# Performance work log

Measured on AMD Instinct MI355X. Metric: run time of the kernel, lower is better.

Reference implementation:

```python
import jax, jax.numpy as jnp
import numpy as np

D = 1024   # dims
H = 16     # heads
HD = D // H  # head_dim = 64
F = HD // 2  # rotary frequency count


def _layernorm(x, g, b, eps=1e-5):
    m = x.mean(-1, keepdims=True)
    v = jnp.mean((x - m) ** 2, axis=-1, keepdims=True)
    return (x - m) * jax.lax.rsqrt(v + eps) * g + b


def _freq_base():
    # mask=None branch of rotary._compute_freqs: mel-style frequencies
    mel_max = 2595.0 * np.log10(1.0 + 4000.0 / 200.0)
    scale = 10.0 ** (np.linspace(0.0, mel_max, F) / 2595.0) - 1.0
    return jnp.asarray(200.0 * scale / 1000.0, dtype=jnp.float32)  # [F]


def _rope_polar(xh, radius, theta):
    # xh: [b,h,c,hd]; radius: [b,c] (learned per-token magnitude); theta: [c,F]
    # complex multiply of interleaved pairs by r*exp(i*theta)
    b_, h_, c_, hd_ = xh.shape
    xp = xh.reshape(b_, h_, c_, F, 2)
    xr, xi = xp[..., 0], xp[..., 1]
    cos = jnp.cos(theta)[None, None]  # [1,1,c,F]
    sin = jnp.sin(theta)[None, None]
    r = radius[:, None, :, None]      # [b,1,c,1]
    out_r = r * (xr * cos - xi * sin)
    out_i = r * (xr * sin + xi * cos)
    return jnp.stack([out_r, out_i], axis=-1).reshape(b_, h_, c_, hd_)


def setup_inputs() -> dict:
    key = jax.random.key(0)
    ks = jax.random.split(key, 6)
    B, C = 2, 2048
    s = 0.02
    return {
        "x": jax.random.normal(ks[0], (B, C, D), jnp.float32),
        "ln_q_g": jnp.ones((D,), jnp.float32),
        "ln_q_b": jnp.zeros((D,), jnp.float32),
        "Wq": jax.random.normal(ks[1], (D, D), jnp.float32) * s,
        "bq": jnp.zeros((D,), jnp.float32),
        "ln_kv_g": jnp.ones((D,), jnp.float32),
        "ln_kv_b": jnp.zeros((D,), jnp.float32),
        "Wkv": jax.random.normal(ks[2], (D, 2 * D), jnp.float32) * s,
        "bkv": jnp.zeros((2 * D,), jnp.float32),
        "Wout": jax.random.normal(ks[3], (D, D), jnp.float32) * s,
        "bout": jnp.zeros((D,), jnp.float32),
        "lnh_g": jnp.ones((HD,), jnp.float32),
        "lnh_b": jnp.zeros((HD,), jnp.float32),
        "Wr": jax.random.normal(ks[4], (D, 1), jnp.float32) * s,
        "br": jnp.zeros((1,), jnp.float32),
    }


def reference(x, ln_q_g, ln_q_b, Wq, bq, ln_kv_g, ln_kv_b, Wkv, bkv,
              Wout, bout, lnh_g, lnh_b, Wr, br):
    B, C, _ = x.shape
    # q path: norm -> linear -> [b,h,c,d]
    q = (_layernorm(x, ln_q_g, ln_q_b) @ Wq + bq).reshape(B, C, H, HD).transpose(0, 2, 1, 3)
    # kv path: norm -> linear -> [2,b,h,c,d]
    kv = (_layernorm(x, ln_kv_g, ln_kv_b) @ Wkv + bkv).reshape(B, C, 2, H, HD).transpose(2, 0, 3, 1, 4)
    k, v = kv[0], kv[1]
    # polar RoPE with learned per-token radius (xa = x for both q and k)
    t = jnp.arange(C, dtype=jnp.float32)
    theta = t[:, None] * _freq_base()[None, :]               # [C,F]
    per_step = (x @ Wr + br)[..., 0]                         # [B,C]
    radius = jnp.clip(per_step / 100.0, 0.5, 2.0)
    q = _rope_polar(q, radius, theta)
    k = _rope_polar(k, radius, theta)
    # per-head LayerNorm fused into SDPA inputs
    qn = _layernorm(q, lnh_g, lnh_b)
    kn = _layernorm(k, lnh_g, lnh_b)
    # non-causal SDPA (torch default scale = 1/sqrt(head_dim))
    logits = jnp.einsum('bhqd,bhkd->bhqk', qn, kn) / jnp.sqrt(jnp.float32(HD))
    attn = jax.nn.softmax(logits, axis=-1)
    o = jnp.einsum('bhqk,bhkd->bhqd', attn, v)
    o = o.transpose(0, 2, 1, 3).reshape(B, C, D)
    return o @ Wout + bout
```

## Files before the change

kernel.cpp:

```cpp
#include <hip/hip_runtime.h>
#include <math.h>

#define D_MODEL 1024
#define NHEADS  16
#define HEADD   64
#define NFREQ   32
#define BATCH   2
#define CSEQ    2048
#define NROWS   (BATCH*CSEQ)

typedef _Float16 half8  __attribute__((ext_vector_type(8)));
typedef _Float16 half4v __attribute__((ext_vector_type(4)));
typedef float    f32x4  __attribute__((ext_vector_type(4)));

__device__ __forceinline__ void async16(void* lds, const void* g)
{
    __builtin_amdgcn_global_load_lds((const __attribute__((address_space(1))) unsigned int*)g,
                                     (__attribute__((address_space(3))) unsigned int*)lds,
                                     16, 0, 0);
}

__global__ __launch_bounds__(256) void build_cs_kernel(float2* __restrict__ cs)
{
    int i = blockIdx.x * 256 + threadIdx.x;
    if (i >= CSEQ * NFREQ) return;
    int c = i >> 5, f = i & (NFREQ - 1);
    double mel_max = 2595.0 * log10(21.0);
    double step    = mel_max / (double)(NFREQ - 1);
    double freq    = 200.0 * (pow(10.0, step * (double)f / 2595.0) - 1.0) / 1000.0;
    float fr = (float)freq;
    float th = (float)c * fr;
    float s, co;
    sincosf(th, &s, &co);
    cs[i] = make_float2(co, s);
}

__global__ __launch_bounds__(256) void transpose_cast_kernel(
    const float* __restrict__ in, _Float16* __restrict__ out, int R, int C)
{
    __shared__ float t[32][33];
    int bx = blockIdx.x * 32;
    int by = blockIdx.y * 32;
    int tx = threadIdx.x, ty = threadIdx.y;
    #pragma unroll
    for (int i = ty; i < 32; i += 8)
        t[i][tx] = in[(size_t)(by + i) * C + bx + tx];
    __syncthreads();
    #pragma unroll
    for (int i = ty; i < 32; i += 8)
        out[(size_t)(bx + i) * R + by + tx] = (_Float16)t[tx][i];
}

__global__ __launch_bounds__(256) void ln_radius_kernel(
    const float* __restrict__ x,
    const float* __restrict__ gq,  const float* __restrict__ bq,
    const float* __restrict__ gkv, const float* __restrict__ bkv,
    const float* __restrict__ Wr,  const float* __restrict__ br,
    _Float16* __restrict__ xq, _Float16* __restrict__ xkv,
    float* __restrict__ radius)
{
    int row = blockIdx.x;
    int tid = threadIdx.x;
    float4 xv = ((const float4*)(x + (size_t)row * D_MODEL))[tid];
    float4 wv = ((const float4*)Wr)[tid];
    float s  = xv.x + xv.y + xv.z + xv.w;
    float ss = xv.x*xv.x + xv.y*xv.y + xv.z*xv.z + xv.w*xv.w;
    float dr = xv.x*wv.x + xv.y*wv.y + xv.z*wv.z + xv.w*wv.w;
    #pragma unroll
    for (int off = 1; off < 64; off <<= 1) {
        s  += __shfl_xor(s, off);
        ss += __shfl_xor(ss, off);
        dr += __shfl_xor(dr, off);
    }
    __shared__ float red[3][4];
    int w = tid >> 6, lane = tid & 63;
    if (lane == 0) { red[0][w] = s; red[1][w] = ss; red[2][w] = dr; }
    __syncthreads();
    s  = red[0][0] + red[0][1] + red[0][2] + red[0][3];
    ss = red[1][0] + red[1][1] + red[1][2] + red[1][3];
    float mean = s * (1.f / D_MODEL);
    float var  = ss * (1.f / D_MODEL) - mean * mean;
    float rinv = rsqrtf(var + 1e-5f);
    float4 gqv = ((const float4*)gq)[tid],  bqv = ((const float4*)bq)[tid];
    float4 gkv4= ((const float4*)gkv)[tid], bkv4= ((const float4*)bkv)[tid];
    float xn0 = (xv.x - mean) * rinv, xn1 = (xv.y - mean) * rinv;
    float xn2 = (xv.z - mean) * rinv, xn3 = (xv.w - mean) * rinv;
    half4v q4 = { (_Float16)(xn0*gqv.x + bqv.x), (_Float16)(xn1*gqv.y + bqv.y),
                  (_Float16)(xn2*gqv.z + bqv.z), (_Float16)(xn3*gqv.w + bqv.w) };
    half4v k4 = { (_Float16)(xn0*gkv4.x + bkv4.x), (_Float16)(xn1*gkv4.y + bkv4.y),
                  (_Float16)(xn2*gkv4.z + bkv4.z), (_Float16)(xn3*gkv4.w + bkv4.w) };
    *(half4v*)&xq [(size_t)row * D_MODEL + tid * 4] = q4;
    *(half4v*)&xkv[(size_t)row * D_MODEL + tid * 4] = k4;
    if (tid == 0) {
        float drt = red[2][0] + red[2][1] + red[2][2] + red[2][3];
        float p = (drt + br[0]) * 0.01f;
        radius[row] = fminf(fmaxf(p, 0.5f), 2.0f);
    }
}

__device__ __forceinline__ void gemm_core64(
    const _Float16* __restrict__ A, const _Float16* __restrict__ B,
    int bm, int bn, int K, _Float16* As, _Float16* Bs, f32x4 (*acc)[4])
{
    int tid = threadIdx.x, lane = tid & 63, w = tid >> 6;
    int wm = w >> 1, wn = w & 1;
    int l15 = lane & 15, lg = lane >> 4;
    int sr8 = lane >> 3;
    int csrc = (lane & 7) ^ sr8;

    auto stage = [&](int buf, int k0) {
        #pragma unroll
        for (int i = 0; i < 4; ++i) {
            int seg = w * 4 + i;
            int row = seg * 8 + sr8;
            async16(&As[buf * 8192 + seg * 512], &A[(size_t)(bm + row) * K + k0 + csrc * 8]);
            async16(&Bs[buf * 8192 + seg * 512], &B[(size_t)(bn + row) * K + k0 + csrc * 8]);
        }
    };

    stage(0, 0);
    __syncthreads();
    int cur = 0;
    for (int k0 = 0; k0 < K; k0 += 64) {
        if (k0 + 64 < K) stage(cur ^ 1, k0 + 64);
        #pragma unroll
        for (int ks = 0; ks < 2; ++ks) {
            half8 af[4], bf[4];
            #pragma unroll
            for (int m = 0; m < 4; ++m) {
                int row = wm * 64 + m * 16 + l15;
                af[m] = *(const half8*)&As[cur * 8192 + row * 64 + ((ks * 4 + lg) ^ (row & 7)) * 8];
            }
            #pragma unroll
            for (int n = 0; n < 4; ++n) {
                int row = wn * 64 + n * 16 + l15;
                bf[n] = *(const half8*)&Bs[cur * 8192 + row * 64 + ((ks * 4 + lg) ^ (row & 7)) * 8];
            }
            #pragma unroll
            for (int m = 0; m < 4; ++m)
                #pragma unroll
                for (int n = 0; n < 4; ++n)
                    acc[m][n] = __builtin_amdgcn_mfma_f32_16x16x32_f16(af[m], bf[n], acc[m][n], 0, 0, 0);
        }
        __syncthreads();
        cur ^= 1;
    }
}

__global__ __launch_bounds__(256) void gemm_qkv_kernel(
    const _Float16* __restrict__ xq,  const _Float16* __restrict__ xkv,
    const _Float16* __restrict__ WqT, const _Float16* __restrict__ WkvT,
    const float* __restrict__ bq,     const float* __restrict__ bkv,
    const float* __restrict__ radius, const float2* __restrict__ cs_tab,
    const float* __restrict__ lnh_g,  const float* __restrict__ lnh_b,
    _Float16* __restrict__ qn, _Float16* __restrict__ kn, _Float16* __restrict__ v_rm)
{
    __shared__ _Float16 As[2 * 8192];
    __shared__ _Float16 Bs[2 * 8192];
    int orig = blockIdx.x;
    int wg = (orig & 7) * 96 + (orig >> 3);

    const _Float16 *A, *Bt;
    const float* bias;
    int bm, bn;
    bool isq;
    if (wg < 256) { isq = true;  A = xq;  Bt = WqT;  bias = bq;
                    bm = (wg >> 3) * 128;  bn = (wg & 7) * 128; }
    else          { int t = wg - 256; isq = false; A = xkv; Bt = WkvT; bias = bkv;
                    bm = (t >> 4) * 128;   bn = (t & 15) * 128; }

    f32x4 acc[4][4];
    f32x4 z = {0.f, 0.f, 0.f, 0.f};
    #pragma unroll
    for (int m = 0; m < 4; ++m)
        #pragma unroll
        for (int n = 0; n < 4; ++n) acc[m][n] = z;

    gemm_core64(A, Bt, bm, bn, D_MODEL, As, Bs, acc);

    int tid = threadIdx.x, lane = tid & 63, w = tid >> 6;
    int wm = w >> 1, wn = w & 1;
    int l15 = lane & 15, lg = lane >> 4;
    int colbase = bn + wn * 64;

    float bb4[4];
    #pragma unroll
    for (int n = 0; n < 4; ++n) bb4[n] = bias[colbase + n * 16 + l15];

    if (!isq && colbase >= D_MODEL) {
        int vcolb = colbase - D_MODEL;
        #pragma unroll
        for (int m = 0; m < 4; ++m)
            #pragma unroll
            for (int r = 0; r < 4; ++r) {
                int row = bm + wm * 64 + m * 16 + lg * 4 + r;
                #pragma unroll
                for (int n = 0; n < 4; ++n)
                    v_rm[(size_t)row * D_MODEL + vcolb + n * 16 + l15] =
                        (_Float16)(acc[m][n][r] + bb4[n]);
            }
        return;
    }

    float g4[4], bh4[4];
    #pragma unroll
    for (int n = 0; n < 4; ++n) {
        g4[n]  = lnh_g[n * 16 + l15];
        bh4[n] = lnh_b[n * 16 + l15];
    }
    int h = colbase >> 6;
    _Float16* dst = isq ? qn : kn;
    float qs = isq ? 0.125f : 1.f;
    bool im = (l15 & 1) != 0;

    #pragma unroll
    for (int m = 0; m < 4; ++m)
        #pragma unroll
        for (int r = 0; r < 4; ++r) {
            int row = bm + wm * 64 + m * 16 + lg * 4 + r;
            int b = row >> 11, c = row & (CSEQ - 1);
            float rr = radius[row];
            float vals[4];
            float s = 0.f, ss = 0.f;
            #pragma unroll
            for (int n = 0; n < 4; ++n) {
                float v0 = acc[m][n][r] + bb4[n];
                float pr = __shfl_xor(v0, 1);
                float2 cs = cs_tab[c * NFREQ + ((n * 16 + l15) >> 1)];
                float xr_ = im ? pr : v0;
                float xi_ = im ? v0 : pr;
                float rot = im ? rr * (xr_ * cs.y + xi_ * cs.x)
                               : rr * (xr_ * cs.x - xi_ * cs.y);
                vals[n] = rot;
                s += rot; ss += rot * rot;
            }
            #pragma unroll
            for (int off = 1; off < 16; off <<= 1) {
                s  += __shfl_xor(s, off);
                ss += __shfl_xor(ss, off);
            }
            float mean = s * (1.f / 64.f);
            float var  = ss * (1.f / 64.f) - mean * mean;
            float ri   = rsqrtf(var + 1e-5f);
            size_t base = ((size_t)(b * NHEADS + h) * CSEQ + c) * HEADD;
            #pragma unroll
            for (int n = 0; n < 4; ++n) {
                float o = ((vals[n] - mean) * ri * g4[n] + bh4[n]) * qs;
                dst[base + n * 16 + l15] = (_Float16)o;
            }
        }
}

__global__ __launch_bounds__(256) void gemm_out_kernel(
    const _Float16* __restrict__ A, const _Float16* __restrict__ BT,
    const float* __restrict__ bias, float* __restrict__ C)
{
    __shared__ _Float16 As[2 * 8192];
    __shared__ _Float16 Bs[2 * 8192];
    int orig = blockIdx.x;
    int wg = (orig & 7) * 32 + (orig >> 3);
    int bm = (wg >> 3) * 128;
    int bn = (wg & 7) * 128;

    f32x4 acc[4][4];
    f32x4 z = {0.f, 0.f, 0.f, 0.f};
    #pragma unroll
    for (int m = 0; m < 4; ++m)
        #pragma unroll
        for (int n = 0; n < 4; ++n) acc[m][n] = z;

    gemm_core64(A, BT, bm, bn, D_MODEL, As, Bs, acc);

    int tid = threadIdx.x, lane = tid & 63, w = tid >> 6;
    int wm = w >> 1, wn = w & 1;
    int l15 = lane & 15, lg = lane >> 4;
    #pragma unroll
    for (int m = 0; m < 4; ++m) {
        int row = bm + wm * 64 + m * 16 + lg * 4;
        #pragma unroll
        for (int n = 0; n < 4; ++n) {
            int col = bn + wn * 64 + n * 16 + l15;
            float bb = bias[col];
            #pragma unroll
            for (int r = 0; r < 4; ++r)
                C[(size_t)(row + r) * D_MODEL + col] = acc[m][n][r] + bb;
        }
    }
}

__global__ __launch_bounds__(256) void v_transpose_f16(
    const _Float16* __restrict__ v_rm, _Float16* __restrict__ vT)
{
    int bh = blockIdx.x >> 5;
    int c0 = (blockIdx.x & 31) * 64;
    int b = bh >> 4, h = bh & 15;
    __shared__ _Float16 t[64][68];
    int tid = threadIdx.x;
    int dcol = tid & 63, quarter = tid >> 6;
    for (int c = quarter; c < 64; c += 4)
        t[c][dcol] = v_rm[(size_t)(b * CSEQ + c0 + c) * D_MODEL + h * HEADD + dcol];
    __syncthreads();
    for (int d = quarter; d < 64; d += 4)
        vT[(size_t)(bh * HEADD + d) * CSEQ + c0 + dcol] = t[dcol][d];
}

#define KVB 64
#define NT  (CSEQ / KVB)

__global__ __launch_bounds__(256, 4) void attn_kernel(
    const _Float16* __restrict__ qn, const _Float16* __restrict__ kn,
    const _Float16* __restrict__ vT, _Float16* __restrict__ o)
{
    __shared__ _Float16 KsB[2][KVB * 64];
    __shared__ _Float16 VsB[2][KVB * 64];
    __shared__ _Float16 P[4][16 * 64];
    int tid = threadIdx.x, lane = tid & 63, w = tid >> 6;
    int l15 = lane & 15, lg = lane >> 4;

    int orig = blockIdx.x;
    int wg   = (orig & 7) * 128 + (orig >> 3);
    int bh   = wg >> 5;
    int qc   = wg & 31;
    int q0   = qc * 64 + w * 16;

    const _Float16* qh = qn + (size_t)bh * CSEQ * HEADD;
    const _Float16* kh = kn + (size_t)bh * CSEQ * HEADD;
    const _Float16* vh = vT + (size_t)bh * HEADD * CSEQ;

    half8 aq[2];
    #pragma unroll
    for (int ks = 0; ks < 2; ++ks)
        aq[ks] = *(const half8*)&qh[(size_t)(q0 + l15) * HEADD + ks * 32 + lg * 8];

    f32x4 z = {0.f, 0.f, 0.f, 0.f};
    f32x4 oacc[4];
    #pragma unroll
    for (int d4 = 0; d4 < 4; ++d4) oacc[d4] = z;
    float mrun = -1e30f, lrun = 0.f;

    int srow_in = lane >> 3;
    int csrc    = (lane & 7) ^ srow_in;
    int lsw     = l15 & 7;

    auto stage = [&](int buf, int kt) {
        int k0 = kt * KVB;
        #pragma unroll
        for (int i = 0; i < 2; ++i) {
            int seg = w * 2 + i;
            int r = seg * 8 + srow_in;
            async16(&KsB[buf][seg * 512], &kh[(size_t)(k0 + r) * HEADD + csrc * 8]);
            async16(&VsB[buf][seg * 512], &vh[(size_t)r * CSEQ + k0 + csrc * 8]);
        }
    };

    stage(0, 0);
    __syncthreads();
    int cur = 0;

    for (int kt = 0; kt < NT; ++kt) {
        if (kt + 1 < NT) stage(cur ^ 1, kt + 1);

        f32x4 st[4];
        #pragma unroll
        for (int n = 0; n < 4; ++n) st[n] = z;
        #pragma unroll
        for (int ks = 0; ks < 2; ++ks) {
            half8 ak[4];
            #pragma unroll
            for (int n = 0; n < 4; ++n) {
                int row = n * 16 + l15;
                int ch = (ks * 4 + lg) ^ (row & 7);
                ak[n] = *(const half8*)&KsB[cur][row * 64 + ch * 8];
            }
            #pragma unroll
            for (int n = 0; n < 4; ++n)
                st[n] = __builtin_amdgcn_mfma_f32_16x16x32_f16(ak[n], aq[ks], st[n], 0, 0, 0);
        }

        float mx0 = fmaxf(fmaxf(st[0][0], st[0][1]), fmaxf(st[0][2], st[0][3]));
        float mx1 = fmaxf(fmaxf(st[1][0], st[1][1]), fmaxf(st[1][2], st[1][3]));
        float mx2 = fmaxf(fmaxf(st[2][0], st[2][1]), fmaxf(st[2][2], st[2][3]));
        float mx3 = fmaxf(fmaxf(st[3][0], st[3][1]), fmaxf(st[3][2], st[3][3]));
        float tmax = fmaxf(fmaxf(mx0, mx1), fmaxf(mx2, mx3));
        tmax = fmaxf(tmax, __shfl_xor(tmax, 16));
        tmax = fmaxf(tmax, __shfl_xor(tmax, 32));

        if (!__all(tmax <= mrun + 8.f)) {
            float nm = fmaxf(mrun, tmax);
            float sc = __expf(mrun - nm);
            mrun = nm;
            lrun *= sc;
            float scO[4];
            #pragma unroll
            for (int r = 0; r < 4; ++r) scO[r] = __shfl(sc, lg * 4 + r);
            #pragma unroll
            for (int d4 = 0; d4 < 4; ++d4)
                #pragma unroll
                for (int r = 0; r < 4; ++r) oacc[d4][r] *= scO[r];
        }

        float ps = 0.f;
        #pragma unroll
        for (int n = 0; n < 4; ++n)
            #pragma unroll
            for (int r = 0; r < 4; ++r) {
                float e = __expf(st[n][r] - mrun);
                st[n][r] = e;
                ps += e;
            }
        ps += __shfl_xor(ps, 16);
        ps += __shfl_xor(ps, 32);
        lrun += ps;

        #pragma unroll
        for (int n = 0; n < 4; ++n) {
            half4v pk;
            #pragma unroll
            for (int r = 0; r < 4; ++r) pk[r] = (_Float16)st[n][r];
            int t  = n * 2 + (lg >> 1);
            int tp = t ^ lsw;
            *(half4v*)&P[w][l15 * 64 + tp * 8 + (lg & 1) * 4] = pk;
        }

        #pragma unroll
        for (int ks = 0; ks < 2; ++ks) {
            int tp2 = (ks * 4 + lg) ^ lsw;
            half8 ap = *(const half8*)&P[w][l15 * 64 + tp2 * 8];
            half8 bv[4];
            #pragma unroll
            for (int d4 = 0; d4 < 4; ++d4) {
                int row = d4 * 16 + l15;
                int ch = (ks * 4 + lg) ^ (row & 7);
                bv[d4] = *(const half8*)&VsB[cur][row * 64 + ch * 8];
            }
            #pragma unroll
            for (int d4 = 0; d4 < 4; ++d4)
                oacc[d4] = __builtin_amdgcn_mfma_f32_16x16x32_f16(ap, bv[d4], oacc[d4], 0, 0, 0);
        }

        __syncthreads();
        cur ^= 1;
    }

    int b = bh >> 4, h = bh & 15;
    #pragma unroll
    for (int r = 0; r < 4; ++r) {
        float lr = __shfl(lrun, lg * 4 + r);
        float inv = 1.f / lr;
        int c = q0 + lg * 4 + r;
        size_t base = ((size_t)b * CSEQ + c) * D_MODEL + h * HEADD;
        #pragma unroll
        for (int d4 = 0; d4 < 4; ++d4)
            o[base + d4 * 16 + l15] = (_Float16)(oacc[d4][r] * inv);
    }
}

extern "C" void kernel_launch(void* const* d_in, const int* in_sizes, int n_in,
                              void* d_out, int out_size, void* d_ws, size_t ws_size,
                              hipStream_t stream)
{
    (void)in_sizes; (void)n_in; (void)out_size; (void)ws_size;
    const float* x      = (const float*)d_in[0];
    const float* ln_q_g = (const float*)d_in[1];
    const float* ln_q_b = (const float*)d_in[2];
    const float* Wq     = (const float*)d_in[3];
    const float* bq     = (const float*)d_in[4];
    const float* ln_kv_g= (const float*)d_in[5];
    const float* ln_kv_b= (const float*)d_in[6];
    const float* Wkv    = (const float*)d_in[7];
    const float* bkv    = (const float*)d_in[8];
    const float* Wout   = (const float*)d_in[9];
    const float* bout   = (const float*)d_in[10];
    const float* lnh_g  = (const float*)d_in[11];
    const float* lnh_b  = (const float*)d_in[12];
    const float* Wr     = (const float*)d_in[13];
    const float* br     = (const float*)d_in[14];
    float* out = (float*)d_out;

    char* ws = (char*)d_ws;
    size_t off = 0;
    auto alloc = [&](size_t bytes) -> void* {
        void* p = ws + off;
        off += (bytes + 255) & ~(size_t)255;
        return p;
    };
    _Float16* WqT   = (_Float16*)alloc((size_t)D_MODEL * D_MODEL * 2);
    _Float16* WkvT  = (_Float16*)alloc((size_t)2 * D_MODEL * D_MODEL * 2);
    _Float16* WoutT = (_Float16*)alloc((size_t)D_MODEL * D_MODEL * 2);
    float*    radius= (float*)   alloc((size_t)NROWS * 4);
    float2*   cs_tab= (float2*)  alloc((size_t)CSEQ * NFREQ * 8);
    _Float16* vT    = (_Float16*)alloc((size_t)BATCH * NHEADS * HEADD * CSEQ * 2);
    _Float16* v_rm  = (_Float16*)alloc((size_t)NROWS * D_MODEL * 2);
    _Float16* xq    = (_Float16*)alloc((size_t)NROWS * D_MODEL * 2);
    _Float16* xkv   = (_Float16*)alloc((size_t)NROWS * D_MODEL * 2);
    _Float16* qn    = (_Float16*)alloc((size_t)NROWS * D_MODEL * 2);
    _Float16* kn    = (_Float16*)alloc((size_t)NROWS * D_MODEL * 2);
    _Float16* o_h   = (_Float16*)alloc((size_t)NROWS * D_MODEL * 2);

    hipLaunchKernelGGL(build_cs_kernel, dim3(CSEQ * NFREQ / 256), dim3(256), 0, stream, cs_tab);
    hipLaunchKernelGGL(transpose_cast_kernel, dim3(D_MODEL/32, D_MODEL/32), dim3(32, 8), 0, stream,
                       Wq, WqT, D_MODEL, D_MODEL);
    hipLaunchKernelGGL(transpose_cast_kernel, dim3(2*D_MODEL/32, D_MODEL/32), dim3(32, 8), 0, stream,
                       Wkv, WkvT, D_MODEL, 2*D_MODEL);
    hipLaunchKernelGGL(transpose_cast_kernel, dim3(D_MODEL/32, D_MODEL/32), dim3(32, 8), 0, stream,
                       Wout, WoutT, D_MODEL, D_MODEL);
    hipLaunchKernelGGL(ln_radius_kernel, dim3(NROWS), dim3(256), 0, stream,
                       x, ln_q_g, ln_q_b, ln_kv_g, ln_kv_b, Wr, br, xq, xkv, radius);
    hipLaunchKernelGGL(gemm_qkv_kernel, dim3(768), dim3(256), 0, stream,
                       xq, xkv, WqT, WkvT, bq, bkv, radius, cs_tab, lnh_g, lnh_b,
                       qn, kn, v_rm);
    hipLaunchKernelGGL(v_transpose_f16, dim3(BATCH*NHEADS*CSEQ/64), dim3(256), 0, stream,
                       v_rm, vT);
    hipLaunchKernelGGL(attn_kernel, dim3(BATCH*NHEADS*CSEQ/64), dim3(256), 0, stream,
                       qn, kn, vT, o_h);
    hipLaunchKernelGGL(gemm_out_kernel, dim3(256), dim3(256), 0, stream,
                       o_h, WoutT, bout, out);
}
```

Measured before the change: 162.2 us.

## Fold LayerNorm affine into QKV weights and shrink GEMM K-tile to 32

Result: faster. 157.5 us (-2.9%).

```diff
diff --git a/kernel.cpp b/kernel.cpp
--- a/kernel.cpp
+++ b/kernel.cpp
@@ -8,6 +8,7 @@
 #define BATCH   2
 #define CSEQ    2048
 #define NROWS   (BATCH*CSEQ)
+#define NQKV    (3*D_MODEL)
 
 typedef _Float16 half8  __attribute__((ext_vector_type(8)));
 typedef _Float16 half4v __attribute__((ext_vector_type(4)));
@@ -35,10 +36,21 @@
     cs[i] = make_float2(co, s);
 }
 
-__global__ __launch_bounds__(256) void transpose_cast_kernel(
-    const float* __restrict__ in, _Float16* __restrict__ out, int R, int C)
+__global__ __launch_bounds__(256) void bias_init_kernel(
+    const float* __restrict__ bq, const float* __restrict__ bkv, float* __restrict__ be)
+{
+    int i = blockIdx.x * 256 + threadIdx.x;
+    if (i < D_MODEL) be[i] = bq[i];
+    else if (i < NQKV) be[i] = bkv[i - D_MODEL];
+}
+
+__global__ __launch_bounds__(256) void transpose_fold_kernel(
+    const float* __restrict__ in, _Float16* __restrict__ out, int R, int C,
+    int rowoff, const float* __restrict__ scale,
+    const float* __restrict__ bfold, float* __restrict__ bias_acc)
 {
     __shared__ float t[32][33];
+    __shared__ float part[4][32];
     int bx = blockIdx.x * 32;
     int by = blockIdx.y * 32;
     int tx = threadIdx.x, ty = threadIdx.y;
@@ -46,18 +58,28 @@
     for (int i = ty; i < 32; i += 8)
         t[i][tx] = in[(size_t)(by + i) * C + bx + tx];
     __syncthreads();
+    float sc = scale ? scale[by + tx] : 1.f;
     #pragma unroll
     for (int i = ty; i < 32; i += 8)
-        out[(size_t)(bx + i) * R + by + tx] = (_Float16)t[tx][i];
+        out[(size_t)(rowoff + bx + i) * R + by + tx] = (_Float16)(t[tx][i] * sc);
+    if (bfold) {
+        float p = 0.f;
+        #pragma unroll
+        for (int i = ty; i < 32; i += 8)
+            p += bfold[by + i] * t[i][tx];
+        p += __shfl_xor(p, 32);
+        if ((ty & 1) == 0) part[ty >> 1][tx] = p;
+        __syncthreads();
+        if (ty == 0)
+            atomicAdd(&bias_acc[rowoff + bx + tx],
+                      part[0][tx] + part[1][tx] + part[2][tx] + part[3][tx]);
+    }
 }
 
 __global__ __launch_bounds__(256) void ln_radius_kernel(
     const float* __restrict__ x,
-    const float* __restrict__ gq,  const float* __restrict__ bq,
-    const float* __restrict__ gkv, const float* __restrict__ bkv,
     const float* __restrict__ Wr,  const float* __restrict__ br,
-    _Float16* __restrict__ xq, _Float16* __restrict__ xkv,
-    float* __restrict__ radius)
+    _Float16* __restrict__ xn, float* __restrict__ radius)
 {
     int row = blockIdx.x;
     int tid = threadIdx.x;
@@ -81,16 +103,9 @@
     float mean = s * (1.f / D_MODEL);
     float var  = ss * (1.f / D_MODEL) - mean * mean;
     float rinv = rsqrtf(var + 1e-5f);
-    float4 gqv = ((const float4*)gq)[tid],  bqv = ((const float4*)bq)[tid];
-    float4 gkv4= ((const float4*)gkv)[tid], bkv4= ((const float4*)bkv)[tid];
-    float xn0 = (xv.x - mean) * rinv, xn1 = (xv.y - mean) * rinv;
-    float xn2 = (xv.z - mean) * rinv, xn3 = (xv.w - mean) * rinv;
-    half4v q4 = { (_Float16)(xn0*gqv.x + bqv.x), (_Float16)(xn1*gqv.y + bqv.y),
-                  (_Float16)(xn2*gqv.z + bqv.z), (_Float16)(xn3*gqv.w + bqv.w) };
-    half4v k4 = { (_Float16)(xn0*gkv4.x + bkv4.x), (_Float16)(xn1*gkv4.y + bkv4.y),
-                  (_Float16)(xn2*gkv4.z + bkv4.z), (_Float16)(xn3*gkv4.w + bkv4.w) };
-    *(half4v*)&xq [(size_t)row * D_MODEL + tid * 4] = q4;
-    *(half4v*)&xkv[(size_t)row * D_MODEL + tid * 4] = k4;
+    half4v o4 = { (_Float16)((xv.x - mean) * rinv), (_Float16)((xv.y - mean) * rinv),
+                  (_Float16)((xv.z - mean) * rinv), (_Float16)((xv.w - mean) * rinv) };
+    *(half4v*)&xn[(size_t)row * D_MODEL + tid * 4] = o4;
     if (tid == 0) {
         float drt = red[2][0] + red[2][1] + red[2][2] + red[2][3];
         float p = (drt + br[0]) * 0.01f;
@@ -98,76 +113,61 @@
     }
 }
 
-__device__ __forceinline__ void gemm_core64(
+__device__ __forceinline__ void gemm_core32(
     const _Float16* __restrict__ A, const _Float16* __restrict__ B,
     int bm, int bn, int K, _Float16* As, _Float16* Bs, f32x4 (*acc)[4])
 {
     int tid = threadIdx.x, lane = tid & 63, w = tid >> 6;
     int wm = w >> 1, wn = w & 1;
     int l15 = lane & 15, lg = lane >> 4;
-    int sr8 = lane >> 3;
-    int csrc = (lane & 7) ^ sr8;
+    int sr  = lane >> 2;
+    int sch = lane & 3;
 
     auto stage = [&](int buf, int k0) {
         #pragma unroll
-        for (int i = 0; i < 4; ++i) {
-            int seg = w * 4 + i;
-            int row = seg * 8 + sr8;
-            async16(&As[buf * 8192 + seg * 512], &A[(size_t)(bm + row) * K + k0 + csrc * 8]);
-            async16(&Bs[buf * 8192 + seg * 512], &B[(size_t)(bn + row) * K + k0 + csrc * 8]);
+        for (int i = 0; i < 2; ++i) {
+            int seg = w * 2 + i;
+            int row = seg * 16 + sr;
+            async16(&As[buf * 4096 + seg * 512], &A[(size_t)(bm + row) * K + k0 + sch * 8]);
+            async16(&Bs[buf * 4096 + seg * 512], &B[(size_t)(bn + row) * K + k0 + sch * 8]);
         }
     };
 
     stage(0, 0);
     __syncthreads();
     int cur = 0;
-    for (int k0 = 0; k0 < K; k0 += 64) {
-        if (k0 + 64 < K) stage(cur ^ 1, k0 + 64);
-        #pragma unroll
-        for (int ks = 0; ks < 2; ++ks) {
-            half8 af[4], bf[4];
-            #pragma unroll
-            for (int m = 0; m < 4; ++m) {
-                int row = wm * 64 + m * 16 + l15;
-                af[m] = *(const half8*)&As[cur * 8192 + row * 64 + ((ks * 4 + lg) ^ (row & 7)) * 8];
-            }
-            #pragma unroll
-            for (int n = 0; n < 4; ++n) {
-                int row = wn * 64 + n * 16 + l15;
-                bf[n] = *(const half8*)&Bs[cur * 8192 + row * 64 + ((ks * 4 + lg) ^ (row & 7)) * 8];
-            }
-            #pragma unroll
-            for (int m = 0; m < 4; ++m)
-                #pragma unroll
-                for (int n = 0; n < 4; ++n)
-                    acc[m][n] = __builtin_amdgcn_mfma_f32_16x16x32_f16(af[m], bf[n], acc[m][n], 0, 0, 0);
-        }
+    for (int k0 = 0; k0 < K; k0 += 32) {
+        if (k0 + 32 < K) stage(cur ^ 1, k0 + 32);
+        half8 af[4], bf[4];
+        #pragma unroll
+        for (int m = 0; m < 4; ++m)
+            af[m] = *(const half8*)&As[cur * 4096 + (wm * 64 + m * 16 + l15) * 32 + lg * 8];
+        #pragma unroll
+        for (int n = 0; n < 4; ++n)
+            bf[n] = *(const half8*)&Bs[cur * 4096 + (wn * 64 + n * 16 + l15) * 32 + lg * 8];
+        #pragma unroll
+        for (int m = 0; m < 4; ++m)
+            #pragma unroll
+            for (int n = 0; n < 4; ++n)
+                acc[m][n] = __builtin_amdgcn_mfma_f32_16x16x32_f16(af[m], bf[n], acc[m][n], 0, 0, 0);
         __syncthreads();
         cur ^= 1;
     }
 }
 
-__global__ __launch_bounds__(256) void gemm_qkv_kernel(
-    const _Float16* __restrict__ xq,  const _Float16* __restrict__ xkv,
-    const _Float16* __restrict__ WqT, const _Float16* __restrict__ WkvT,
-    const float* __restrict__ bq,     const float* __restrict__ bkv,
+__global__ __launch_bounds__(256, 4) void gemm_qkv_kernel(
+    const _Float16* __restrict__ xn,  const _Float16* __restrict__ WT,
+    const float* __restrict__ bias_eff,
     const float* __restrict__ radius, const float2* __restrict__ cs_tab,
     const float* __restrict__ lnh_g,  const float* __restrict__ lnh_b,
     _Float16* __restrict__ qn, _Float16* __restrict__ kn, _Float16* __restrict__ v_rm)
 {
-    __shared__ _Float16 As[2 * 8192];
-    __shared__ _Float16 Bs[2 * 8192];
+    __shared__ _Float16 As[2 * 4096];
+    __shared__ _Float16 Bs[2 * 4096];
     int orig = blockIdx.x;
     int wg = (orig & 7) * 96 + (orig >> 3);
-
-    const _Float16 *A, *Bt;
-    const float* bias;
-    int bm, bn;
-    bool isq;
-    if (wg < 256) { isq = true;  A = xq;  Bt = WqT;  bias = bq;
-                    bm = (wg >> 3) * 128;  bn = (wg & 7) * 128; }
-    else          { int t = wg - 256; isq = false; A = xkv; Bt = WkvT; bias = bkv;
-                    bm = (t >> 4) * 128;   bn = (t & 15) * 128; }
+    int bm = (wg / 24) * 128;
+    int bn = (wg % 24) * 128;
 
     f32x4 acc[4][4];
     f32x4 z = {0.f, 0.f, 0.f, 0.f};
@@ -176,7 +176,7 @@
         #pragma unroll
         for (int n = 0; n < 4; ++n) acc[m][n] = z;
 
-    gemm_core64(A, Bt, bm, bn, D_MODEL, As, Bs, acc);
+    gemm_core32(xn, WT, bm, bn, D_MODEL, As, Bs, acc);
 
     int tid = threadIdx.x, lane = tid & 63, w = tid >> 6;
     int wm = w >> 1, wn = w & 1;
@@ -185,10 +185,10 @@
 
     float bb4[4];
     #pragma unroll
-    for (int n = 0; n < 4; ++n) bb4[n] = bias[colbase + n * 16 + l15];
-
-    if (!isq && colbase >= D_MODEL) {
-        int vcolb = colbase - D_MODEL;
+    for (int n = 0; n < 4; ++n) bb4[n] = bias_eff[colbase + n * 16 + l15];
+
+    if (colbase >= 2 * D_MODEL) {
+        int vcolb = colbase - 2 * D_MODEL;
         #pragma unroll
         for (int m = 0; m < 4; ++m)
             #pragma unroll
@@ -202,16 +202,18 @@
         return;
     }
 
+    bool isq = colbase < D_MODEL;
+    int h = (colbase & (D_MODEL - 1)) >> 6;
+    _Float16* dst = isq ? qn : kn;
+    float qs = isq ? 0.125f : 1.f;
+    bool im = (l15 & 1) != 0;
+
     float g4[4], bh4[4];
     #pragma unroll
     for (int n = 0; n < 4; ++n) {
         g4[n]  = lnh_g[n * 16 + l15];
         bh4[n] = lnh_b[n * 16 + l15];
     }
-    int h = colbase >> 6;
-    _Float16* dst = isq ? qn : kn;
-    float qs = isq ? 0.125f : 1.f;
-    bool im = (l15 & 1) != 0;
 
     #pragma unroll
     for (int m = 0; m < 4; ++m)
@@ -251,12 +253,12 @@
         }
 }
 
-__global__ __launch_bounds__(256) void gemm_out_kernel(
+__global__ __launch_bounds__(256, 4) void gemm_out_kernel(
     const _Float16* __restrict__ A, const _Float16* __restrict__ BT,
     const float* __restrict__ bias, float* __restrict__ C)
 {
-    __shared__ _Float16 As[2 * 8192];
-    __shared__ _Float16 Bs[2 * 8192];
+    __shared__ _Float16 As[2 * 4096];
+    __shared__ _Float16 Bs[2 * 4096];
     int orig = blockIdx.x;
     int wg = (orig & 7) * 32 + (orig >> 3);
     int bm = (wg >> 3) * 128;
@@ -269,7 +271,7 @@
         #pragma unroll
         for (int n = 0; n < 4; ++n) acc[m][n] = z;
 
-    gemm_core64(A, BT, bm, bn, D_MODEL, As, Bs, acc);
+    gemm_core32(A, BT, bm, bn, D_MODEL, As, Bs, acc);
 
     int tid = threadIdx.x, lane = tid & 63, w = tid >> 6;
     int wm = w >> 1, wn = w & 1;
@@ -484,31 +486,31 @@
         off += (bytes + 255) & ~(size_t)255;
         return p;
     };
-    _Float16* WqT   = (_Float16*)alloc((size_t)D_MODEL * D_MODEL * 2);
-    _Float16* WkvT  = (_Float16*)alloc((size_t)2 * D_MODEL * D_MODEL * 2);
-    _Float16* WoutT = (_Float16*)alloc((size_t)D_MODEL * D_MODEL * 2);
-    float*    radius= (float*)   alloc((size_t)NROWS * 4);
-    float2*   cs_tab= (float2*)  alloc((size_t)CSEQ * NFREQ * 8);
-    _Float16* vT    = (_Float16*)alloc((size_t)BATCH * NHEADS * HEADD * CSEQ * 2);
-    _Float16* v_rm  = (_Float16*)alloc((size_t)NROWS * D_MODEL * 2);
-    _Float16* xq    = (_Float16*)alloc((size_t)NROWS * D_MODEL * 2);
-    _Float16* xkv   = (_Float16*)alloc((size_t)NROWS * D_MODEL * 2);
-    _Float16* qn    = (_Float16*)alloc((size_t)NROWS * D_MODEL * 2);
-    _Float16* kn    = (_Float16*)alloc((size_t)NROWS * D_MODEL * 2);
-    _Float16* o_h   = (_Float16*)alloc((size_t)NROWS * D_MODEL * 2);
-
+    _Float16* WqkvT  = (_Float16*)alloc((size_t)NQKV * D_MODEL * 2);
+    _Float16* WoutT  = (_Float16*)alloc((size_t)D_MODEL * D_MODEL * 2);
+    float*    bias_e = (float*)   alloc((size_t)NQKV * 4);
+    float*    radius = (float*)   alloc((size_t)NROWS * 4);
+    float2*   cs_tab = (float2*)  alloc((size_t)CSEQ * NFREQ * 8);
+    _Float16* vT     = (_Float16*)alloc((size_t)BATCH * NHEADS * HEADD * CSEQ * 2);
+    _Float16* v_rm   = (_Float16*)alloc((size_t)NROWS * D_MODEL * 2);
+    _Float16* xn     = (_Float16*)alloc((size_t)NROWS * D_MODEL * 2);
+    _Float16* qn     = (_Float16*)alloc((size_t)NROWS * D_MODEL * 2);
+    _Float16* kn     = (_Float16*)alloc((size_t)NROWS * D_MODEL * 2);
+    _Float16* o_h    = (_Float16*)alloc((size_t)NROWS * D_MODEL * 2);
+
+    hipLaunchKernelGGL(bias_init_kernel, dim3(NQKV / 256), dim3(256), 0, stream, bq, bkv, bias_e);
     hipLaunchKernelGGL(build_cs_kernel, dim3(CSEQ * NFREQ / 256), dim3(256), 0, stream, cs_tab);
-    hipLaunchKernelGGL(transpose_cast_kernel, dim3(D_MODEL/32, D_MODEL/32), dim3(32, 8), 0, stream,
-                       Wq, WqT, D_MODEL, D_MODEL);
-    hipLaunchKernelGGL(transpose_cast_kernel, dim3(2*D_MODEL/32, D_MODEL/32), dim3(32, 8), 0, stream,
-                       Wkv, WkvT, D_MODEL, 2*D_MODEL);
-    hipLaunchKernelGGL(transpose_cast_kernel, dim3(D_MODEL/32, D_MODEL/32), dim3(32, 8), 0, stream,
-                       Wout, WoutT, D_MODEL, D_MODEL);
+    hipLaunchKernelGGL(transpose_fold_kernel, dim3(D_MODEL/32, D_MODEL/32), dim3(32, 8), 0, stream,
+                       Wq, WqkvT, D_MODEL, D_MODEL, 0, ln_q_g, ln_q_b, bias_e);
+    hipLaunchKernelGGL(transpose_fold_kernel, dim3(2*D_MODEL/32, D_MODEL/32), dim3(32, 8), 0, stream,
+                       Wkv, WqkvT, D_MODEL, 2*D_MODEL, D_MODEL, ln_kv_g, ln_kv_b, bias_e);
+    hipLaunchKernelGGL(transpose_fold_kernel, dim3(D_MODEL/32, D_MODEL/32), dim3(32, 8), 0, stream,
+                       Wout, WoutT, D_MODEL, D_MODEL, 0, (const float*)nullptr,
+                       (const float*)nullptr, (float*)nullptr);
     hipLaunchKernelGGL(ln_radius_kernel, dim3(NROWS), dim3(256), 0, stream,
-                       x, ln_q_g, ln_q_b, ln_kv_g, ln_kv_b, Wr, br, xq, xkv, radius);
+                       x, Wr, br, xn, radius);
     hipLaunchKernelGGL(gemm_qkv_kernel, dim3(768), dim3(256), 0, stream,
-                       xq, xkv, WqT, WkvT, bq, bkv, radius, cs_tab, lnh_g, lnh_b,
-                       qn, kn, v_rm);
+                       xn, WqkvT, bias_e, radius, cs_tab, lnh_g, lnh_b, qn, kn, v_rm);
     hipLaunchKernelGGL(v_transpose_f16, dim3(BATCH*NHEADS*CSEQ/64), dim3(256), 0, stream,
                        v_rm, vT);
     hipLaunchKernelGGL(attn_kernel, dim3(BATCH*NHEADS*CSEQ/64), dim3(256), 0, stream,
```
